# Kernel optimization log

Hardware: AMD Instinct MI355X
Metric: run time of the kernel (lower is better)

The kernel has to match this reference:

```python
import jax, jax.numpy as jnp
import numpy as np

D_MODEL = 2048
N_HEADS = 16
HEAD_DIM = D_MODEL // N_HEADS


def setup_inputs() -> dict:
    key = jax.random.key(0)
    ks = jax.random.split(key, 5)
    b, l, d = 2, 2048, D_MODEL
    x = jax.random.normal(ks[0], (b, l, d), dtype=jnp.float32)
    # torch nn.Linear weights: y = x @ W.T + b, W shape [out, in]
    s_qkv = 1.0 / np.sqrt(d)
    W_qkv = jax.random.uniform(ks[1], (3 * d, d), dtype=jnp.float32, minval=-s_qkv, maxval=s_qkv)
    b_qkv = jax.random.uniform(ks[2], (3 * d,), dtype=jnp.float32, minval=-s_qkv, maxval=s_qkv)
    W_out = jax.random.uniform(ks[3], (d, d), dtype=jnp.float32, minval=-s_qkv, maxval=s_qkv)
    b_out = jax.random.uniform(ks[4], (d,), dtype=jnp.float32, minval=-s_qkv, maxval=s_qkv)
    return {"x": x, "W_qkv": W_qkv, "b_qkv": b_qkv, "W_out": W_out, "b_out": b_out}


def reference(x, W_qkv, b_qkv, W_out, b_out):
    b, l, d = x.shape
    h, e = N_HEADS, HEAD_DIM
    qkv = x @ W_qkv.T + b_qkv                      # [b, l, 3d]
    q, k, v = jnp.split(qkv, 3, axis=-1)
    # split heads: [b, l, h, e]
    q = q.reshape(b, l, h, e)
    k = k.reshape(b, l, h, e)
    v = v.reshape(b, l, h, e)
    scale = 1.0 / jnp.sqrt(jnp.float32(e))
    scores = jnp.einsum('bqhe,bkhe->bhqk', q, k) * scale  # [b, h, l, l]
    # causal mask (is_causal=True)
    causal = jnp.tril(jnp.ones((l, l), dtype=bool))
    scores = jnp.where(causal[None, None], scores, -jnp.inf)
    attn = jax.nn.softmax(scores, axis=-1)          # dropout p=0 -> identity
    out = jnp.einsum('bhqk,bkhe->bqhe', attn, v)    # [b, l, h, e]
    out = out.reshape(b, l, d)                      # merge heads
    out = out @ W_out.T + b_out
    return out
```

## Files before the change

### kernel.cpp

```cpp
#include <hip/hip_runtime.h>
#include <hip/hip_bf16.h>

#define B_ 2
#define L_ 2048
#define D_ 2048
#define H_ 16
#define E_ 128
#define M_ 4096
#define K_ 2048
#define N3_ 6144

typedef __attribute__((ext_vector_type(4))) float f32x4;
typedef short s16x8 __attribute__((ext_vector_type(8)));

__device__ inline void gld_lds16(const void* g, void* l) {
    __builtin_amdgcn_global_load_lds(
        (const __attribute__((address_space(1))) void*)g,
        (__attribute__((address_space(3))) void*)l, 16, 0, 0);
}

__global__ __launch_bounds__(256)
void cast_bf16(const float* __restrict__ in, __hip_bfloat16* __restrict__ out, int n8)
{
    const int i = blockIdx.x * 256 + threadIdx.x;
    if (i >= n8) return;
    const float4 a = ((const float4*)in)[2 * i];
    const float4 b = ((const float4*)in)[2 * i + 1];
    union { __hip_bfloat16 h[8]; uint4 u; } o;
    o.h[0] = __float2bfloat16(a.x); o.h[1] = __float2bfloat16(a.y);
    o.h[2] = __float2bfloat16(a.z); o.h[3] = __float2bfloat16(a.w);
    o.h[4] = __float2bfloat16(b.x); o.h[5] = __float2bfloat16(b.y);
    o.h[6] = __float2bfloat16(b.z); o.h[7] = __float2bfloat16(b.w);
    ((uint4*)out)[i] = o.u;
}

__global__ __launch_bounds__(512, 2)
void gemm_qkv_8ph(const __hip_bfloat16* __restrict__ A,
                  const __hip_bfloat16* __restrict__ W,
                  const float* __restrict__ bias,
                  __hip_bfloat16* __restrict__ q,
                  __hip_bfloat16* __restrict__ k,
                  __hip_bfloat16* __restrict__ vT)
{
    __shared__ char lds[131072];

    const int t    = threadIdx.x;
    const int lane = t & 63;
    const int w    = t >> 6;
    const int l15  = lane & 15;
    const int hi   = lane >> 4;
    const int wr   = w >> 2;
    const int wc   = w & 3;
    const int n0   = blockIdx.x << 8;
    const int m0   = blockIdx.y << 8;

    f32x4 acc[8][4];
    const f32x4 z4 = {0.f, 0.f, 0.f, 0.f};
    #pragma unroll
    for (int m = 0; m < 8; ++m)
        #pragma unroll
        for (int n = 0; n < 4; ++n) acc[m][n] = z4;
    s16x8 afr[4][2], bfr[4][2];

    const __hip_bfloat16* Abase = A + (size_t)m0 * K_;
    const __hip_bfloat16* Wbase = W + (size_t)n0 * K_;

    auto stage_half = [&](const __hip_bfloat16* src, char* dst) {
        #pragma unroll
        for (int i = 0; i < 2; ++i) {
            const int slot = (i << 9) + t;
            const int row  = slot >> 3;
            const int csw  = (slot & 7) ^ (row & 7);
            gld_lds16(src + (size_t)row * K_ + (csw << 3),
                      dst + (i << 13) + (w << 10));
        }
    };

    stage_half(Abase,                     lds);
    stage_half(Abase + (size_t)128 * K_,  lds + 16384);
    stage_half(Wbase,                     lds + 32768);
    stage_half(Wbase + (size_t)128 * K_,  lds + 49152);
    __syncthreads();

    const int NT = K_ / 64;
    for (int T = 0; T < NT; ++T) {
        const int  cur = T & 1;
        const char* Al = lds + cur * 65536;
        const char* Bl = Al + 32768;
        char*       An = lds + (cur ^ 1) * 65536;
        char*       Bn = An + 32768;
        const __hip_bfloat16* Asrc = Abase + (size_t)(T + 1) * 64;
        const __hip_bfloat16* Wsrc = Wbase + (size_t)(T + 1) * 64;
        const bool pf = (T + 1 < NT);

        auto lda = [&](int m, int kk) {
            const int row = (wr << 7) + (m << 4) + l15;
            const int ch  = ((kk << 2) + hi) ^ (row & 7);
            return *(const s16x8*)(Al + row * 128 + (ch << 4));
        };
        auto ldb = [&](int n, int kk) {
            const int row = (wc << 6) + (n << 4) + l15;
            const int ch  = ((kk << 2) + hi) ^ (row & 7);
            return *(const s16x8*)(Bl + row * 128 + (ch << 4));
        };

        #pragma unroll
        for (int m = 0; m < 4; ++m) { afr[m][0] = lda(m, 0); afr[m][1] = lda(m, 1); }
        #pragma unroll
        for (int n = 0; n < 2; ++n) { bfr[n][0] = ldb(n, 0); bfr[n][1] = ldb(n, 1); }
        if (pf) stage_half(Asrc, An);
        __builtin_amdgcn_s_barrier();
        __builtin_amdgcn_s_setprio(1);
        #pragma unroll
        for (int kk = 0; kk < 2; ++kk)
            #pragma unroll
            for (int n = 0; n < 2; ++n)
                #pragma unroll
                for (int m = 0; m < 4; ++m)
                    acc[m][n] = __builtin_amdgcn_mfma_f32_16x16x32_bf16(
                        afr[m][kk], bfr[n][kk], acc[m][n], 0, 0, 0);
        __builtin_amdgcn_s_setprio(0);
        __builtin_amdgcn_s_barrier();

        #pragma unroll
        for (int n = 0; n < 2; ++n) { bfr[2 + n][0] = ldb(2 + n, 0); bfr[2 + n][1] = ldb(2 + n, 1); }
        if (pf) stage_half(Asrc + (size_t)128 * K_, An + 16384);
        __builtin_amdgcn_s_barrier();
        __builtin_amdgcn_s_setprio(1);
        #pragma unroll
        for (int kk = 0; kk < 2; ++kk)
            #pragma unroll
            for (int n = 0; n < 2; ++n)
                #pragma unroll
                for (int m = 0; m < 4; ++m)
                    acc[m][2 + n] = __builtin_amdgcn_mfma_f32_16x16x32_bf16(
                        afr[m][kk], bfr[2 + n][kk], acc[m][2 + n], 0, 0, 0);
        __builtin_amdgcn_s_setprio(0);
        __builtin_amdgcn_s_barrier();

        #pragma unroll
        for (int m = 0; m < 4; ++m) { afr[m][0] = lda(4 + m, 0); afr[m][1] = lda(4 + m, 1); }
        if (pf) stage_half(Wsrc, Bn);
        __builtin_amdgcn_s_barrier();
        __builtin_amdgcn_s_setprio(1);
        #pragma unroll
        for (int kk = 0; kk < 2; ++kk)
            #pragma unroll
            for (int n = 0; n < 2; ++n)
                #pragma unroll
                for (int m = 0; m < 4; ++m)
                    acc[4 + m][2 + n] = __builtin_amdgcn_mfma_f32_16x16x32_bf16(
                        afr[m][kk], bfr[2 + n][kk], acc[4 + m][2 + n], 0, 0, 0);
        __builtin_amdgcn_s_setprio(0);
        __builtin_amdgcn_s_barrier();

        if (pf) stage_half(Wsrc + (size_t)128 * K_, Bn + 16384);
        __builtin_amdgcn_s_barrier();
        __builtin_amdgcn_s_setprio(1);
        #pragma unroll
        for (int kk = 0; kk < 2; ++kk)
            #pragma unroll
            for (int n = 0; n < 2; ++n)
                #pragma unroll
                for (int m = 0; m < 4; ++m)
                    acc[4 + m][n] = __builtin_amdgcn_mfma_f32_16x16x32_bf16(
                        afr[m][kk], bfr[n][kk], acc[4 + m][n], 0, 0, 0);
        __builtin_amdgcn_s_setprio(0);
        __syncthreads();
    }

    #pragma unroll
    for (int n = 0; n < 4; ++n) {
        const int col   = n0 + (wc << 6) + (n << 4) + l15;
        const int which = col >> 11;
        const int h     = (col >> 7) & 15;
        const int e     = col & 127;
        const float bn  = bias[col];
        #pragma unroll
        for (int m = 0; m < 8; ++m) {
            const int rowb = m0 + (wr << 7) + (m << 4) + (hi << 2);
            #pragma unroll
            for (int i = 0; i < 4; ++i) {
                const int mm = rowb + i;
                const int b  = mm >> 11;
                const int l  = mm & 2047;
                const __hip_bfloat16 val = __float2bfloat16(acc[m][n][i] + bn);
                if (which == 0)
                    q[((size_t)((b * H_ + h) * L_ + l) << 7) + e] = val;
                else if (which == 1)
                    k[((size_t)((b * H_ + h) * L_ + l) << 7) + e] = val;
                else
                    vT[(((size_t)(b * H_ + h) << 7) + e) * L_ + l] = val;
            }
        }
    }
}

__global__ __launch_bounds__(256)
void gemm_bf16_nt(const __hip_bfloat16* __restrict__ A,
                  const __hip_bfloat16* __restrict__ W,
                  const float* __restrict__ bias,
                  float* __restrict__ o)
{
    __shared__ __hip_bfloat16 As[128 * 32];
    __shared__ __hip_bfloat16 Bs[128 * 32];

    const int t    = threadIdx.x;
    const int lane = t & 63;
    const int w    = t >> 6;
    const int l15  = lane & 15;
    const int hi   = lane >> 4;
    const int wr   = w >> 1, wc = w & 1;
    const int m0   = blockIdx.y << 7;
    const int n0   = blockIdx.x << 7;

    f32x4 acc[4][4];
    const f32x4 z4 = {0.f, 0.f, 0.f, 0.f};
    #pragma unroll
    for (int m = 0; m < 4; ++m)
        #pragma unroll
        for (int n = 0; n < 4; ++n) acc[m][n] = z4;

    const __hip_bfloat16* Ab = A + (size_t)m0 * K_;
    const __hip_bfloat16* Bb = W + (size_t)n0 * K_;
    const int srow = t >> 2;
    const int sc   = (t & 3) << 3;

    for (int k0 = 0; k0 < K_; k0 += 32) {
        #pragma unroll
        for (int j = 0; j < 2; ++j) {
            gld_lds16(Ab + (size_t)(j * 64 + srow) * K_ + k0 + sc,
                      (char*)As + j * 4096 + w * 1024);
            gld_lds16(Bb + (size_t)(j * 64 + srow) * K_ + k0 + sc,
                      (char*)Bs + j * 4096 + w * 1024);
        }
        __syncthreads();
        s16x8 af[4], bf[4];
        #pragma unroll
        for (int m = 0; m < 4; ++m)
            af[m] = *(const s16x8*)(As + (wr * 64 + m * 16 + l15) * 32 + hi * 8);
        #pragma unroll
        for (int n = 0; n < 4; ++n)
            bf[n] = *(const s16x8*)(Bs + (wc * 64 + n * 16 + l15) * 32 + hi * 8);
        #pragma unroll
        for (int m = 0; m < 4; ++m)
            #pragma unroll
            for (int n = 0; n < 4; ++n)
                acc[m][n] = __builtin_amdgcn_mfma_f32_16x16x32_bf16(af[m], bf[n], acc[m][n], 0, 0, 0);
        __syncthreads();
    }

    #pragma unroll
    for (int n = 0; n < 4; ++n) {
        const int col = n0 + wc * 64 + n * 16 + l15;
        const float bn = bias[col];
        #pragma unroll
        for (int m = 0; m < 4; ++m) {
            const int rowb = m0 + wr * 64 + m * 16 + hi * 4;
            #pragma unroll
            for (int i = 0; i < 4; ++i)
                o[(size_t)(rowb + i) * D_ + col] = acc[m][n][i] + bn;
        }
    }
}

__global__ __launch_bounds__(256)
void attn_mfma(const __hip_bfloat16* __restrict__ Qg,
               const __hip_bfloat16* __restrict__ Kg,
               const __hip_bfloat16* __restrict__ vTg,
               __hip_bfloat16* __restrict__ O)
{
    __shared__ __hip_bfloat16 Ks[2][64 * 128];
    __shared__ __hip_bfloat16 Vt[2][128 * 64];
    __shared__ __hip_bfloat16 Ps[4 * 1024];

    const int t    = threadIdx.x;
    const int lane = t & 63;
    const int w    = t >> 6;
    const int l15  = lane & 15;
    const int hi   = lane >> 4;
    const int pq   = blockIdx.x;
    const int bh   = blockIdx.y;
    const size_t base = (size_t)bh * (L_ * E_);
    const float scale = 0.08838834764831843f;
    const int krow = t >> 4;
    const int kc16 = t & 15;

    const __hip_bfloat16* Kbh  = Kg  + base;
    const __hip_bfloat16* vTbh = vTg + base;

    auto stage = [&](int kt2, int buf) {
        const __hip_bfloat16* Kb = Kbh + ((size_t)(kt2 << 6)) * E_;
        char* kd = (char*)Ks + buf * 16384 + (w << 10);
        #pragma unroll
        for (int j = 0; j < 4; ++j) {
            const int row = (j << 4) + krow;
            const int csw = kc16 ^ (row & 7);
            gld_lds16(Kb + (size_t)row * E_ + (csw << 3), kd + (j << 12));
        }
        const __hip_bfloat16* Vb = vTbh + (kt2 << 6);
        char* vd = (char*)Vt + buf * 16384 + (w << 10);
        #pragma unroll
        for (int j = 0; j < 4; ++j) {
            const int e  = (j << 5) + (t >> 3);
            const int g8 = (t & 7) ^ (e & 7);
            gld_lds16(Vb + (size_t)e * L_ + (g8 << 3), vd + (j << 12));
        }
    };

    const f32x4 z4 = {0.f, 0.f, 0.f, 0.f};

    #pragma unroll 1
    for (int seg = 0; seg < 2; ++seg) {
        const int qt = seg ? pq : 31 - pq;
        const int q0 = (qt << 6) + (w << 4);

        s16x8 qf[4];
        #pragma unroll
        for (int e0 = 0; e0 < 4; ++e0)
            qf[e0] = *(const s16x8*)(Qg + base + (size_t)(q0 + l15) * E_ + e0 * 32 + hi * 8);

        f32x4 oacc[8];
        #pragma unroll
        for (int ef = 0; ef < 8; ++ef) oacc[ef] = z4;
        float mrow[4] = {-1e30f, -1e30f, -1e30f, -1e30f};
        float lrow[4] = {0.f, 0.f, 0.f, 0.f};

        stage(0, 0);
        __syncthreads();

        for (int kt = 0; kt <= qt; ++kt) {
            const int cur = kt & 1;
            if (kt < qt) stage(kt + 1, cur ^ 1);

            const char* Ksc = (const char*)Ks + cur * 16384;
            const char* Vtc = (const char*)Vt + cur * 16384;

            f32x4 sf[4];
            #pragma unroll
            for (int c = 0; c < 4; ++c) {
                f32x4 s = z4;
                const int row = (c << 4) + l15;
                #pragma unroll
                for (int e0 = 0; e0 < 4; ++e0) {
                    const int ch = ((e0 << 2) + hi) ^ (row & 7);
                    const s16x8 kf = *(const s16x8*)(Ksc + (row << 8) + (ch << 4));
                    s = __builtin_amdgcn_mfma_f32_16x16x32_bf16(qf[e0], kf, s, 0, 0, 0);
                }
                sf[c] = s;
            }

            float p4[4][4];
            float tmax[4] = {-1e30f, -1e30f, -1e30f, -1e30f};
            if (kt == qt) {
                const int qg = q0 + (hi << 2);
                #pragma unroll
                for (int c = 0; c < 4; ++c) {
                    const int kvg = (kt << 6) + (c << 4) + l15;
                    #pragma unroll
                    for (int i = 0; i < 4; ++i) {
                        float s = sf[c][i] * scale;
                        if (kvg > qg + i) s = -1e30f;
                        p4[c][i] = s;
                        tmax[i] = fmaxf(tmax[i], s);
                    }
                }
            } else {
                #pragma unroll
                for (int c = 0; c < 4; ++c)
                    #pragma unroll
                    for (int i = 0; i < 4; ++i) {
                        const float s = sf[c][i] * scale;
                        p4[c][i] = s;
                        tmax[i] = fmaxf(tmax[i], s);
                    }
            }
            float fsc[4];
            #pragma unroll
            for (int i = 0; i < 4; ++i) {
                float v = tmax[i];
                v = fmaxf(v, __shfl_xor(v, 1));
                v = fmaxf(v, __shfl_xor(v, 2));
                v = fmaxf(v, __shfl_xor(v, 4));
                v = fmaxf(v, __shfl_xor(v, 8));
                const float mnew = fmaxf(mrow[i], v);
                fsc[i] = __expf(mrow[i] - mnew);
                mrow[i] = mnew;
                float sum = 0.f;
                #pragma unroll
                for (int c = 0; c < 4; ++c) {
                    const float pe = __expf(p4[c][i] - mnew);
                    p4[c][i] = pe;
                    sum += pe;
                }
                sum += __shfl_xor(sum, 1);
                sum += __shfl_xor(sum, 2);
                sum += __shfl_xor(sum, 4);
                sum += __shfl_xor(sum, 8);
                lrow[i] = lrow[i] * fsc[i] + sum;
            }
            #pragma unroll
            for (int ef = 0; ef < 8; ++ef)
                #pragma unroll
                for (int i = 0; i < 4; ++i) oacc[ef][i] *= fsc[i];

            #pragma unroll
            for (int c = 0; c < 4; ++c)
                #pragma unroll
                for (int i = 0; i < 4; ++i) {
                    const int r   = (hi << 2) + i;
                    const int col = (c << 4) + l15;
                    const int ch  = (col >> 3) ^ (r & 7);
                    const int by  = (r << 7) + ((ch << 4) | ((col & 7) << 1));
                    *(__hip_bfloat16*)((char*)Ps + (w << 11) + by) = __float2bfloat16(p4[c][i]);
                }
            asm volatile("s_waitcnt lgkmcnt(0)" ::: "memory");

            #pragma unroll
            for (int kh = 0; kh < 2; ++kh) {
                const int chp = ((kh << 2) + hi) ^ (l15 & 7);
                const s16x8 pa = *(const s16x8*)((char*)Ps + (w << 11) + (l15 << 7) + (chp << 4));
                #pragma unroll
                for (int ef = 0; ef < 8; ++ef) {
                    const int e   = (ef << 4) + l15;
                    const int chv = ((kh << 2) + hi) ^ (e & 7);
                    const s16x8 vb = *(const s16x8*)(Vtc + (e << 7) + (chv << 4));
                    oacc[ef] = __builtin_amdgcn_mfma_f32_16x16x32_bf16(pa, vb, oacc[ef], 0, 0, 0);
                }
            }
            __syncthreads();
        }

        const int b = bh >> 4, h = bh & 15;
        float invl[4];
        #pragma unroll
        for (int i = 0; i < 4; ++i) invl[i] = 1.f / lrow[i];
        #pragma unroll
        for (int ef = 0; ef < 8; ++ef) {
            const int e = (ef << 4) + l15;
            #pragma unroll
            for (int i = 0; i < 4; ++i) {
                const int row = q0 + (hi << 2) + i;
                O[((size_t)(b * L_ + row) * D_) + (h << 7) + e] =
                    __float2bfloat16(oacc[ef][i] * invl[i]);
            }
        }
    }
}

extern "C" void kernel_launch(void* const* d_in, const int* in_sizes, int n_in,
                              void* d_out, int out_size, void* d_ws, size_t ws_size,
                              hipStream_t stream)
{
    const float* x    = (const float*)d_in[0];
    const float* Wqkv = (const float*)d_in[1];
    const float* bqkv = (const float*)d_in[2];
    const float* Wout = (const float*)d_in[3];
    const float* bout = (const float*)d_in[4];
    float* out = (float*)d_out;

    __hip_bfloat16* xb  = (__hip_bfloat16*)d_ws;
    __hip_bfloat16* wqb = xb  + (size_t)M_ * K_;
    __hip_bfloat16* wob = wqb + (size_t)N3_ * K_;
    __hip_bfloat16* qb  = wob + (size_t)D_ * K_;
    __hip_bfloat16* kb  = qb  + (size_t)M_ * D_;
    __hip_bfloat16* vtb = kb  + (size_t)M_ * D_;
    __hip_bfloat16* aob = vtb + (size_t)M_ * D_;

    cast_bf16<<<(M_ * K_ / 8) / 256, 256, 0, stream>>>(x, xb, M_ * K_ / 8);
    cast_bf16<<<(N3_ * K_ / 8) / 256, 256, 0, stream>>>(Wqkv, wqb, N3_ * K_ / 8);
    cast_bf16<<<(D_ * K_ / 8) / 256, 256, 0, stream>>>(Wout, wob, D_ * K_ / 8);

    dim3 g1(N3_ / 256, M_ / 256);
    gemm_qkv_8ph<<<g1, dim3(512), 0, stream>>>(xb, wqb, bqkv, qb, kb, vtb);

    dim3 g2(16, B_ * H_);
    attn_mfma<<<g2, dim3(256), 0, stream>>>(qb, kb, vtb, aob);

    dim3 g3(D_ / 128, M_ / 128);
    gemm_bf16_nt<<<g3, dim3(256), 0, stream>>>(aob, wob, bout, out);
}
```

Before: 427.4 us.

## Remap QKV GEMM warps to quadrant tiles with fine-grained vmcnt waits

```diff
diff --git a/kernel.cpp b/kernel.cpp
--- a/kernel.cpp
+++ b/kernel.cpp
@@ -54,13 +54,20 @@
     const int n0   = blockIdx.x << 8;
     const int m0   = blockIdx.y << 8;
 
-    f32x4 acc[8][4];
+    f32x4 acc[2][2][4][2];
     const f32x4 z4 = {0.f, 0.f, 0.f, 0.f};
     #pragma unroll
-    for (int m = 0; m < 8; ++m)
-        #pragma unroll
-        for (int n = 0; n < 4; ++n) acc[m][n] = z4;
-    s16x8 afr[4][2], bfr[4][2];
+    for (int qr = 0; qr < 2; ++qr)
+        #pragma unroll
+        for (int qc = 0; qc < 2; ++qc)
+            #pragma unroll
+            for (int m = 0; m < 4; ++m)
+                #pragma unroll
+                for (int n = 0; n < 2; ++n) acc[qr][qc][m][n] = z4;
+
+    s16x8 afr[4][2];
+    s16x8 bfr0[2][2];
+    s16x8 bfr1[2][2];
 
     const __hip_bfloat16* Abase = A + (size_t)m0 * K_;
     const __hip_bfloat16* Wbase = W + (size_t)n0 * K_;
@@ -77,10 +84,11 @@
     };
 
     stage_half(Abase,                     lds);
+    stage_half(Wbase,                     lds + 32768);
     stage_half(Abase + (size_t)128 * K_,  lds + 16384);
-    stage_half(Wbase,                     lds + 32768);
     stage_half(Wbase + (size_t)128 * K_,  lds + 49152);
-    __syncthreads();
+    asm volatile("s_waitcnt vmcnt(4)" ::: "memory");
+    __builtin_amdgcn_s_barrier();
 
     const int NT = K_ / 64;
     for (int T = 0; T < NT; ++T) {
@@ -93,21 +101,21 @@
         const __hip_bfloat16* Wsrc = Wbase + (size_t)(T + 1) * 64;
         const bool pf = (T + 1 < NT);
 
-        auto lda = [&](int m, int kk) {
-            const int row = (wr << 7) + (m << 4) + l15;
-            const int ch  = ((kk << 2) + hi) ^ (row & 7);
-            return *(const s16x8*)(Al + row * 128 + (ch << 4));
+        auto lda = [&](const char* half, int m, int kk) {
+            const int r  = (wr << 6) + (m << 4) + l15;
+            const int ch = ((kk << 2) + hi) ^ (r & 7);
+            return *(const s16x8*)(half + r * 128 + (ch << 4));
         };
-        auto ldb = [&](int n, int kk) {
-            const int row = (wc << 6) + (n << 4) + l15;
-            const int ch  = ((kk << 2) + hi) ^ (row & 7);
-            return *(const s16x8*)(Bl + row * 128 + (ch << 4));
+        auto ldb = [&](const char* half, int n, int kk) {
+            const int r  = (wc << 5) + (n << 4) + l15;
+            const int ch = ((kk << 2) + hi) ^ (r & 7);
+            return *(const s16x8*)(half + r * 128 + (ch << 4));
         };
 
         #pragma unroll
-        for (int m = 0; m < 4; ++m) { afr[m][0] = lda(m, 0); afr[m][1] = lda(m, 1); }
-        #pragma unroll
-        for (int n = 0; n < 2; ++n) { bfr[n][0] = ldb(n, 0); bfr[n][1] = ldb(n, 1); }
+        for (int m = 0; m < 4; ++m) { afr[m][0]  = lda(Al, m, 0);      afr[m][1]  = lda(Al, m, 1); }
+        #pragma unroll
+        for (int n = 0; n < 2; ++n) { bfr0[n][0] = ldb(Bl, n, 0);      bfr0[n][1] = ldb(Bl, n, 1); }
         if (pf) stage_half(Asrc, An);
         __builtin_amdgcn_s_barrier();
         __builtin_amdgcn_s_setprio(1);
@@ -117,13 +125,31 @@
             for (int n = 0; n < 2; ++n)
                 #pragma unroll
                 for (int m = 0; m < 4; ++m)
-                    acc[m][n] = __builtin_amdgcn_mfma_f32_16x16x32_bf16(
-                        afr[m][kk], bfr[n][kk], acc[m][n], 0, 0, 0);
+                    acc[0][0][m][n] = __builtin_amdgcn_mfma_f32_16x16x32_bf16(
+                        afr[m][kk], bfr0[n][kk], acc[0][0][m][n], 0, 0, 0);
         __builtin_amdgcn_s_setprio(0);
-        __builtin_amdgcn_s_barrier();
-
-        #pragma unroll
-        for (int n = 0; n < 2; ++n) { bfr[2 + n][0] = ldb(2 + n, 0); bfr[2 + n][1] = ldb(2 + n, 1); }
+        if (pf) asm volatile("s_waitcnt vmcnt(2)" ::: "memory");
+        else    asm volatile("s_waitcnt vmcnt(0)" ::: "memory");
+        __builtin_amdgcn_s_barrier();
+
+        #pragma unroll
+        for (int n = 0; n < 2; ++n) { bfr1[n][0] = ldb(Bl + 16384, n, 0); bfr1[n][1] = ldb(Bl + 16384, n, 1); }
+        if (pf) stage_half(Wsrc, Bn);
+        __builtin_amdgcn_s_barrier();
+        __builtin_amdgcn_s_setprio(1);
+        #pragma unroll
+        for (int kk = 0; kk < 2; ++kk)
+            #pragma unroll
+            for (int n = 0; n < 2; ++n)
+                #pragma unroll
+                for (int m = 0; m < 4; ++m)
+                    acc[0][1][m][n] = __builtin_amdgcn_mfma_f32_16x16x32_bf16(
+                        afr[m][kk], bfr1[n][kk], acc[0][1][m][n], 0, 0, 0);
+        __builtin_amdgcn_s_setprio(0);
+        __builtin_amdgcn_s_barrier();
+
+        #pragma unroll
+        for (int m = 0; m < 4; ++m) { afr[m][0] = lda(Al + 16384, m, 0); afr[m][1] = lda(Al + 16384, m, 1); }
         if (pf) stage_half(Asrc + (size_t)128 * K_, An + 16384);
         __builtin_amdgcn_s_barrier();
         __builtin_amdgcn_s_setprio(1);
@@ -133,14 +159,12 @@
             for (int n = 0; n < 2; ++n)
                 #pragma unroll
                 for (int m = 0; m < 4; ++m)
-                    acc[m][2 + n] = __builtin_amdgcn_mfma_f32_16x16x32_bf16(
-                        afr[m][kk], bfr[2 + n][kk], acc[m][2 + n], 0, 0, 0);
+                    acc[1][1][m][n] = __builtin_amdgcn_mfma_f32_16x16x32_bf16(
+                        afr[m][kk], bfr1[n][kk], acc[1][1][m][n], 0, 0, 0);
         __builtin_amdgcn_s_setprio(0);
         __builtin_amdgcn_s_barrier();
 
-        #pragma unroll
-        for (int m = 0; m < 4; ++m) { afr[m][0] = lda(4 + m, 0); afr[m][1] = lda(4 + m, 1); }
-        if (pf) stage_half(Wsrc, Bn);
+        if (pf) stage_half(Wsrc + (size_t)128 * K_, Bn + 16384);
         __builtin_amdgcn_s_barrier();
         __builtin_amdgcn_s_setprio(1);
         #pragma unroll
@@ -149,51 +173,42 @@
             for (int n = 0; n < 2; ++n)
                 #pragma unroll
                 for (int m = 0; m < 4; ++m)
-                    acc[4 + m][2 + n] = __builtin_amdgcn_mfma_f32_16x16x32_bf16(
-                        afr[m][kk], bfr[2 + n][kk], acc[4 + m][2 + n], 0, 0, 0);
+                    acc[1][0][m][n] = __builtin_amdgcn_mfma_f32_16x16x32_bf16(
+                        afr[m][kk], bfr0[n][kk], acc[1][0][m][n], 0, 0, 0);
         __builtin_amdgcn_s_setprio(0);
-        __builtin_amdgcn_s_barrier();
-
-        if (pf) stage_half(Wsrc + (size_t)128 * K_, Bn + 16384);
-        __builtin_amdgcn_s_barrier();
-        __builtin_amdgcn_s_setprio(1);
-        #pragma unroll
-        for (int kk = 0; kk < 2; ++kk)
-            #pragma unroll
-            for (int n = 0; n < 2; ++n)
-                #pragma unroll
-                for (int m = 0; m < 4; ++m)
-                    acc[4 + m][n] = __builtin_amdgcn_mfma_f32_16x16x32_bf16(
-                        afr[m][kk], bfr[n][kk], acc[4 + m][n], 0, 0, 0);
-        __builtin_amdgcn_s_setprio(0);
-        __syncthreads();
+        if (pf) asm volatile("s_waitcnt vmcnt(4)" ::: "memory");
+        __builtin_amdgcn_s_barrier();
     }
 
     #pragma unroll
-    for (int n = 0; n < 4; ++n) {
-        const int col   = n0 + (wc << 6) + (n << 4) + l15;
-        const int which = col >> 11;
-        const int h     = (col >> 7) & 15;
-        const int e     = col & 127;
-        const float bn  = bias[col];
-        #pragma unroll
-        for (int m = 0; m < 8; ++m) {
-            const int rowb = m0 + (wr << 7) + (m << 4) + (hi << 2);
-            #pragma unroll
-            for (int i = 0; i < 4; ++i) {
-                const int mm = rowb + i;
-                const int b  = mm >> 11;
-                const int l  = mm & 2047;
-                const __hip_bfloat16 val = __float2bfloat16(acc[m][n][i] + bn);
-                if (which == 0)
-                    q[((size_t)((b * H_ + h) * L_ + l) << 7) + e] = val;
-                else if (which == 1)
-                    k[((size_t)((b * H_ + h) * L_ + l) << 7) + e] = val;
-                else
-                    vT[(((size_t)(b * H_ + h) << 7) + e) * L_ + l] = val;
-            }
-        }
-    }
+    for (int qc = 0; qc < 2; ++qc)
+        #pragma unroll
+        for (int n = 0; n < 2; ++n) {
+            const int col   = n0 + (qc << 7) + (wc << 5) + (n << 4) + l15;
+            const int which = col >> 11;
+            const int h     = (col >> 7) & 15;
+            const int e     = col & 127;
+            const float bn  = bias[col];
+            #pragma unroll
+            for (int qr = 0; qr < 2; ++qr)
+                #pragma unroll
+                for (int m = 0; m < 4; ++m) {
+                    const int rowb = m0 + (qr << 7) + (wr << 6) + (m << 4) + (hi << 2);
+                    #pragma unroll
+                    for (int i = 0; i < 4; ++i) {
+                        const int mm = rowb + i;
+                        const int b  = mm >> 11;
+                        const int l  = mm & 2047;
+                        const __hip_bfloat16 val = __float2bfloat16(acc[qr][qc][m][n][i] + bn);
+                        if (which == 0)
+                            q[((size_t)((b * H_ + h) * L_ + l) << 7) + e] = val;
+                        else if (which == 1)
+                            k[((size_t)((b * H_ + h) * L_ + l) << 7) + e] = val;
+                        else
+                            vT[(((size_t)(b * H_ + h) << 7) + e) * L_ + l] = val;
+                    }
+                }
+        }
 }
 
 __global__ __launch_bounds__(256)
```

Measured after the change: 422.5 us. No clear change (-1.1%).
